# Optimization experiments

Measured on AMD Instinct MI355X. Metric: run time of the kernel, lower is better.

Reference implementation:

```python
import jax, jax.numpy as jnp
import numpy as np

N, E, F_IN, H, C = 50000, 800000, 256, 128, 40


def _gcn_norm(edge_index, num_nodes, dtype):
    # add self loops (fill value 1.0), symmetric normalization D^-1/2 A D^-1/2
    src, dst = edge_index[0], edge_index[1]
    loop = jnp.arange(num_nodes, dtype=src.dtype)
    src = jnp.concatenate([src, loop])
    dst = jnp.concatenate([dst, loop])
    w = jnp.ones(src.shape[0], dtype=dtype)
    deg = jax.ops.segment_sum(w, dst, num_segments=num_nodes)
    dinv = jnp.where(deg > 0, jax.lax.rsqrt(deg), jnp.zeros_like(deg))
    norm = dinv[src] * w * dinv[dst]
    return src, dst, norm


def _propagate(x, src, dst, w, num_nodes):
    # gather x[src], scale by edge weight, scatter-add at dst (SpMM)
    return jax.ops.segment_sum(w[:, None] * x[src], dst, num_segments=num_nodes)


def _mixhop_conv(x, src, dst, w, Ws, b):
    # powers = [0, 1, 2]; Ws[p] is [in, out]
    n = x.shape[0]
    outs = [x @ Ws[0]]
    h = x
    for p in (1, 2):
        h = _propagate(h, src, dst, w, n)
        outs.append(h @ Ws[p])
    return jnp.concatenate(outs, axis=-1) + b


def setup_inputs() -> dict:
    key = jax.random.key(0)
    ks = jax.random.split(key, 10)
    x = jax.random.normal(ks[0], (N, F_IN), dtype=jnp.float32)
    edge_index = jax.random.randint(ks[1], (2, E), 0, N, dtype=jnp.int64)
    s1 = 1.0 / np.sqrt(F_IN)
    s2 = 1.0 / np.sqrt(3 * H)
    return {
        "x": x,
        "edge_index": edge_index,
        "W1_0": jax.random.uniform(ks[2], (F_IN, H), jnp.float32, -s1, s1),
        "W1_1": jax.random.uniform(ks[3], (F_IN, H), jnp.float32, -s1, s1),
        "W1_2": jax.random.uniform(ks[4], (F_IN, H), jnp.float32, -s1, s1),
        "b1": jnp.zeros((3 * H,), jnp.float32),
        "W2_0": jax.random.uniform(ks[5], (3 * H, C), jnp.float32, -s2, s2),
        "W2_1": jax.random.uniform(ks[6], (3 * H, C), jnp.float32, -s2, s2),
        "W2_2": jax.random.uniform(ks[7], (3 * H, C), jnp.float32, -s2, s2),
        "b2": jnp.zeros((3 * C,), jnp.float32),
    }


def reference(x, edge_index, W1_0, W1_1, W1_2, b1, W2_0, W2_1, W2_2, b2):
    n = x.shape[0]
    src, dst, w = _gcn_norm(edge_index, n, x.dtype)
    h = jax.nn.relu(_mixhop_conv(x, src, dst, w, (W1_0, W1_1, W1_2), b1))
    # eval mode: dropout is identity
    out = _mixhop_conv(h, src, dst, w, (W2_0, W2_1, W2_2), b2)
    return jax.nn.log_softmax(out, axis=1)
```

## Files before the change

kernel.cpp:

```cpp
#include <hip/hip_runtime.h>
#include <hip/hip_bf16.h>
#include <math.h>

#define N_NODES 50000
#define F_IN 256
#define H1 128
#define C_OUT 40
#define L1W 384
#define L2W 120
#define L2WP 128
#define NBUK 196
#define NBLK1 256

typedef __attribute__((ext_vector_type(8))) short short8;
typedef __attribute__((ext_vector_type(4))) float f32x4;
typedef __attribute__((ext_vector_type(2))) float f32x2;
typedef __attribute__((ext_vector_type(4))) unsigned short us4;

__device__ inline unsigned short f2bf(float f) {
    union { float f; unsigned int u; } x;
    x.f = f;
    unsigned int u = x.u;
    return (unsigned short)((u + 0x7FFF + ((u >> 16) & 1)) >> 16);
}
__device__ inline float bf2f(unsigned short u) {
    union { unsigned int u; float f; } x;
    x.u = (unsigned int)u << 16;
    return x.f;
}
__device__ inline unsigned int pack_fp8x4(float a, float b, float c, float d) {
    int v = 0;
    v = __builtin_amdgcn_cvt_pk_fp8_f32(a, b, v, false);
    v = __builtin_amdgcn_cvt_pk_fp8_f32(c, d, v, true);
    return (unsigned int)v;
}
__device__ inline unsigned char pack_fp8x1(float a) {
    return (unsigned char)(__builtin_amdgcn_cvt_pk_fp8_f32(a, a, 0, false) & 0xFF);
}
#define EDGE_S(r) ((int)((r) & 0xFFFFu))
#define EDGE_W(r) bf2f((unsigned short)((r) >> 16))


__global__ void detect_k(const int* __restrict__ ei, int* __restrict__ flag) {
    __shared__ int any;
    if (threadIdx.x == 0) any = 0;
    __syncthreads();
    int v = 0;
    for (int r = 0; r < 4; r++) {
        int e = threadIdx.x + r * 256;
        v |= ei[e * 2 + 1];
    }
    if (v != 0) atomicOr(&any, 1);
    __syncthreads();
    if (threadIdx.x == 0) *flag = any;
}


__global__ void hist_k(const int* __restrict__ ei, const int* __restrict__ flag,
                       int* __restrict__ cnt, int E) {
    int base = (blockIdx.x * 256 + threadIdx.x) * 4;
    if (base >= E) return;
    if (base + 4 <= E) {
        int d0, d1, d2, d3;
        if (*flag) {
            int4 dv = *(const int4*)(ei + E + base);
            d0 = dv.x; d1 = dv.y; d2 = dv.z; d3 = dv.w;
        } else {
            const long long* e64 = (const long long*)ei;
            longlong2 a = *(const longlong2*)(e64 + E + base);
            longlong2 b = *(const longlong2*)(e64 + E + base + 2);
            d0 = (int)a.x; d1 = (int)a.y; d2 = (int)b.x; d3 = (int)b.y;
        }
        atomicAdd(&cnt[d0], 1);
        atomicAdd(&cnt[d1], 1);
        atomicAdd(&cnt[d2], 1);
        atomicAdd(&cnt[d3], 1);
    } else {
        for (int e = base; e < E; e++) {
            int d = (*flag) ? ei[E + e] : (int)((const long long*)ei)[E + e];
            atomicAdd(&cnt[d], 1);
        }
    }
}


__global__ __launch_bounds__(256) void scan1_k(const int* __restrict__ cnt,
                                               int* __restrict__ bsum, int n) {
    int t = threadIdx.x;
    int i = blockIdx.x * 256 + t;
    int v = (i < n) ? cnt[i] : 0;
    for (int off = 32; off; off >>= 1) v += __shfl_down(v, off, 64);
    __shared__ int ws[4];
    if ((t & 63) == 0) ws[t >> 6] = v;
    __syncthreads();
    if (t == 0) bsum[blockIdx.x] = ws[0] + ws[1] + ws[2] + ws[3];
}

__global__ __launch_bounds__(256) void scan2_k(int* __restrict__ bsum,
                                               int* __restrict__ btot, int nb) {
    __shared__ int s[256];
    int t = threadIdx.x;
    int v = (t < nb) ? bsum[t] : 0;
    s[t] = v;
    __syncthreads();
    for (int off = 1; off < 256; off <<= 1) {
        int u = (t >= off) ? s[t - off] : 0;
        __syncthreads();
        s[t] += u;
        __syncthreads();
    }
    if (t < nb) bsum[t] = s[t] - v;
    if (t == nb - 1) *btot = s[t];
}

__global__ __launch_bounds__(256) void scan3_k(const int* __restrict__ cnt,
                                               const int* __restrict__ bsum,
                                               int* __restrict__ rowptr,
// ... 13 lines not shown
    if (i < n) {
        rowptr[i] = s[t] - v + bsum[blockIdx.x];
        if (dinv) dinv[i] = rsqrtf((float)v + 1.0f);
    }
}


__global__ __launch_bounds__(256) void hist2_k(const int* __restrict__ ei,
                                               const int* __restrict__ flag,
                                               int* __restrict__ cnt2, int E) {
    __shared__ int lcnt[NBUK];
    int t = threadIdx.x, blk = blockIdx.x;
    for (int j = t; j < NBUK; j += 256) lcnt[j] = 0;
    __syncthreads();
    int chunk = (E + NBLK1 - 1) / NBLK1;
    int beg = blk * chunk, end = min(beg + chunk, E);
    bool i32 = (*flag) != 0;
    const long long* e64 = (const long long*)ei;
    for (int e = beg + t; e < end; e += 256) {
        int d = i32 ? ei[E + e] : (int)e64[E + e];
        atomicAdd(&lcnt[d >> 8], 1);
    }
    __syncthreads();
    for (int j = t; j < NBUK; j += 256) cnt2[j * NBLK1 + blk] = lcnt[j];
}

__global__ __launch_bounds__(256) void stage_k(const int* __restrict__ ei,
                                               const int* __restrict__ flag,
                                               const int* __restrict__ off2,
                                               unsigned int* __restrict__ stage, int E) {
    __shared__ int lcur[NBUK];
    int t = threadIdx.x, blk = blockIdx.x;
    for (int j = t; j < NBUK; j += 256) lcur[j] = off2[j * NBLK1 + blk];
    __syncthreads();
    int chunk = (E + NBLK1 - 1) / NBLK1;
    int beg = blk * chunk, end = min(beg + chunk, E);
    bool i32 = (*flag) != 0;
    const long long* e64 = (const long long*)ei;
    for (int e = beg + t; e < end; e += 256) {
        int s, d;
        if (i32) { s = ei[e]; d = ei[E + e]; }
        else { s = (int)e64[e]; d = (int)e64[E + e]; }
        int b = d >> 8;
        int pos = atomicAdd(&lcur[b], 1);
        stage[pos] = ((unsigned int)(d & 255) << 16) | (unsigned int)s;
    }
}

__global__ __launch_bounds__(256) void scatter2_k(const unsigned int* __restrict__ stage,
                                                  const int* __restrict__ off2,
                                                  const int* __restrict__ rowptr,
                                                  const float* __restrict__ dinv,
                                                  unsigned int* __restrict__ csr,
                                                  int E, int n) {
    __shared__ int lfill[256];
    int b = blockIdx.x, t = threadIdx.x;
    int node0 = b << 8;
    int node = node0 + t;
    lfill[t] = (node < n) ? rowptr[node] : 0;
    __syncthreads();
    int segBeg = off2[b * NBLK1];
    int segEnd = (b == NBUK - 1) ? E : off2[(b + 1) * NBLK1];
    for (int e = segBeg + t; e < segEnd; e += 256) {
        unsigned int rec = stage[e];
        int dl = rec >> 16;
        int s = rec & 0xFFFF;
        int d = node0 + dl;
        float w = dinv[s] * dinv[d];
        int pos = atomicAdd(&lfill[dl], 1);
        csr[pos] = ((unsigned int)f2bf(w) << 16) | (unsigned int)s;
    }
}


#define N1PACK ((F_IN / 32) * L1W * 32)
#define N2PACK ((L1W / 32) * L2WP * 32)

__global__ void pack_k(const float* __restrict__ w10, const float* __restrict__ w11,
                       const float* __restrict__ w12, const float* __restrict__ w20,
                       const float* __restrict__ w21, const float* __restrict__ w22,
                       unsigned short* __restrict__ Bp1, unsigned short* __restrict__ Bp2) {
    int idx = blockIdx.x * 256 + threadIdx.x;
    if (idx < N1PACK) {
        int kk = idx & 31;
        int nn = (idx >> 5) % L1W;
        int kt = idx / (L1W * 32);
        int k = kt * 32 + kk;
        int p = nn >> 7, c = nn & 127;
        const float* w = (p == 0) ? w10 : (p == 1) ? w11 : w12;
        Bp1[idx] = f2bf(w[k * H1 + c]);
    } else if (idx < N1PACK + N2PACK) {
        int j = idx - N1PACK;
        int kk = j & 31;
        int nn = (j >> 5) & (L2WP - 1);
        int kt = j >> 12;
        int k = kt * 32 + kk;
        unsigned short v = 0;
        if (nn < L2W) {
            int p = nn / 40, c = nn % 40;
            const float* w = (p == 0) ? w20 : (p == 1) ? w21 : w22;
            v = f2bf(w[k * C_OUT + c]);
        }
        Bp2[j] = v;
    }
}


__global__ __launch_bounds__(256) void mgemm1_k(const float* __restrict__ A,
                                                const unsigned short* __restrict__ Bp,
                                                const float* __restrict__ b1,
                                                unsigned short* __restrict__ Hb,
                                                unsigned char* __restrict__ Y8, int N) {
    int tid = threadIdx.x;
    int wave = tid >> 6, lane = tid & 63;
    int m = lane & 15, kq = lane >> 4;
    int nwg = gridDim.x, bid = blockIdx.x;
    int q = nwg >> 3, r = nwg & 7;
    int xcd = bid & 7, pos = bid >> 3;
    int lb = (xcd < r ? xcd * (q + 1) : r * (q + 1) + (xcd - r) * q) + pos;
    int blkM = lb >> 1, blkN = lb & 1;
    int s0 = blkN * 12;
    int row0 = blkM * 64 + wave * 16;
    int arow = row0 + m;
    if (arow >= N) arow = N - 1;
    const float* Ap = A + (size_t)arow * F_IN + kq * 8;
    const unsigned short* Bw = Bp + (size_t)s0 * 512 + (size_t)m * 32 + (size_t)kq * 8;

    short8 areg[8];
#pragma unroll
    for (int kt = 0; kt < 8; kt++) {
        float4 u = *(const float4*)(Ap + kt * 32);
        float4 v = *(const float4*)(Ap + kt * 32 + 4);
        short8 a;
        a[0] = (short)f2bf(u.x); a[1] = (short)f2bf(u.y);
        a[2] = (short)f2bf(u.z); a[3] = (short)f2bf(u.w);
        a[4] = (short)f2bf(v.x); a[5] = (short)f2bf(v.y);
        a[6] = (short)f2bf(v.z); a[7] = (short)f2bf(v.w);
        areg[kt] = a;
    }

    f32x4 acc[12];
#pragma unroll
    for (int s = 0; s < 12; s++) acc[s] = (f32x4){0.f, 0.f, 0.f, 0.f};

    short8 brA[12], brB[12];
#pragma unroll
    for (int s = 0; s < 12; s++) brA[s] = *(const short8*)(Bw + (size_t)s * 512);

#pragma unroll
    for (int kt = 0; kt < 8; kt++) {
        const unsigned short* Bn = Bw + (size_t)(kt + 1) * (L1W * 32);
        if ((kt & 1) == 0) {
            if (kt < 7) {
#pragma unroll
                for (int s = 0; s < 12; s++) brB[s] = *(const short8*)(Bn + (size_t)s * 512);
            }
#pragma unroll
            for (int s = 0; s < 12; s++)
                acc[s] = __builtin_amdgcn_mfma_f32_16x16x32_bf16(areg[kt], brA[s], acc[s], 0, 0, 0);
        } else {
            if (kt < 7) {
#pragma unroll
                for (int s = 0; s < 12; s++) brA[s] = *(const short8*)(Bn + (size_t)s * 512);
            }
#pragma unroll
            for (int s = 0; s < 12; s++)
                acc[s] = __builtin_amdgcn_mfma_f32_16x16x32_bf16(areg[kt], brB[s], acc[s], 0, 0, 0);
        }
    }

    int crow = row0 + kq * 4;
    if (blkN == 0) {
#pragma unroll
        for (int s = 0; s < 8; s++) {
            int col = s * 16 + m;
            float bias = b1[col];
#pragma unroll
            for (int r2 = 0; r2 < 4; r2++) {
                int row = crow + r2;
                if (row < N) Hb[(size_t)row * L1W + col] = f2bf(fmaxf(acc[s][r2] + bias, 0.f));
            }
        }
#pragma unroll
        for (int r2 = 0; r2 < 4; r2++) {
            int row = crow + r2;
            if (row < N) {
                unsigned int u = pack_fp8x4(acc[8][r2], acc[9][r2], acc[10][r2], acc[11][r2]);
                *(unsigned int*)(Y8 + (size_t)row * 256 + m * 16) = u;
            }
        }
    } else {
#pragma unroll
        for (int r2 = 0; r2 < 4; r2++) {
            int row = crow + r2;
            if (row < N) {
                unsigned int u0 = pack_fp8x4(acc[0][r2], acc[1][r2], acc[2][r2], acc[3][r2]);
                uint2 u12;
                u12.x = pack_fp8x4(acc[4][r2], acc[5][r2], acc[6][r2], acc[7][r2]);
                u12.y = pack_fp8x4(acc[8][r2], acc[9][r2], acc[10][r2], acc[11][r2]);
                *(unsigned int*)(Y8 + (size_t)row * 256 + m * 16 + 4) = u0;
                *(uint2*)(Y8 + (size_t)row * 256 + m * 16 + 8) = u12;
            }
        }
    }
}


__global__ __launch_bounds__(256) void mgemm2_k(const unsigned short* __restrict__ A,
                                                const unsigned short* __restrict__ Bp,
                                                unsigned short* __restrict__ Ub,
                                                unsigned char* __restrict__ U8, int N) {
    int tid = threadIdx.x;
    int wave = tid >> 6, lane = tid & 63;
    int m = lane & 15, kq = lane >> 4;
    int row0 = blockIdx.x * 64 + wave * 16;
    int arow = row0 + m;
    if (arow >= N) arow = N - 1;
    const unsigned short* Ap = A + (size_t)arow * L1W + kq * 8;
    const unsigned short* Bw = Bp + (size_t)m * 32 + (size_t)kq * 8;

    short8 areg[12];
#pragma unroll
    for (int kt = 0; kt < 12; kt++) areg[kt] = *(const short8*)(Ap + kt * 32);

    f32x4 acc[8];
#pragma unroll
    for (int s = 0; s < 8; s++) acc[s] = (f32x4){0.f, 0.f, 0.f, 0.f};

    short8 brA[8], brB[8];
#pragma unroll
    for (int s = 0; s < 8; s++) brA[s] = *(const short8*)(Bw + (size_t)s * 512);

#pragma unroll
    for (int kt = 0; kt < 12; kt++) {
        const unsigned short* Bn = Bw + (size_t)(kt + 1) * (L2WP * 32);
        if ((kt & 1) == 0) {
            if (kt < 11) {
#pragma unroll
                for (int s = 0; s < 8; s++) brB[s] = *(const short8*)(Bn + (size_t)s * 512);
            }
#pragma unroll
            for (int s = 0; s < 8; s++)
                acc[s] = __builtin_amdgcn_mfma_f32_16x16x32_bf16(areg[kt], brA[s], acc[s], 0, 0, 0);
        } else {
            if (kt < 11) {
#pragma unroll
                for (int s = 0; s < 8; s++) brA[s] = *(const short8*)(Bn + (size_t)s * 512);
            }
#pragma unroll
            for (int s = 0; s < 8; s++)
                acc[s] = __builtin_amdgcn_mfma_f32_16x16x32_bf16(areg[kt], brB[s], acc[s], 0, 0, 0);
        }
    }

    int crow = row0 + kq * 4;
#pragma unroll
    for (int s = 0; s < 3; s++) {
        int col = s * 16 + m;
#pragma unroll
        for (int r2 = 0; r2 < 4; r2++) {
            int row = crow + r2;
            if (row < N) Ub[(size_t)row * L2WP + col] = f2bf(acc[s][r2]);
        }
    }
#pragma unroll
    for (int r2 = 0; r2 < 4; r2++) {
        int row = crow + r2;
        if (row < N) {
            uint2 u;
            u.x = pack_fp8x4(acc[0][r2], acc[1][r2], acc[2][r2], acc[3][r2]);
            u.y = pack_fp8x4(acc[4][r2], acc[5][r2], acc[6][r2], acc[7][r2]);
            *(uint2*)(U8 + (size_t)row * 128 + m * 8) = u;
        }
    }
}


__global__ __launch_bounds__(256) void prop256f_k(const unsigned char* __restrict__ Y8,
                                                  unsigned short* __restrict__ Hb,
                                                  unsigned char* __restrict__ T8,
                                                  const int* __restrict__ rowptr,
                                                  const unsigned int* __restrict__ csr,
                                                  const float* __restrict__ dinv,
                                                  const float* __restrict__ b1, int n) {
    int wave = threadIdx.x >> 6, lane = threadIdx.x & 63;
    int i = blockIdx.x * 4 + wave;
    if (i >= n) return;
    int beg = rowptr[i], end = rowptr[i + 1];
    float di = dinv[i];
    const unsigned int* sbase = (const unsigned int*)Y8 + lane;
    unsigned int sv = sbase[(size_t)i * 64];
    float w = di * di;
    f32x2 slo = __builtin_amdgcn_cvt_pk_f32_fp8(sv, false);
    f32x2 shi = __builtin_amdgcn_cvt_pk_f32_fp8(sv, true);
    float a0 = w * slo.x, a1 = w * slo.y, a2 = w * shi.x, a3 = w * shi.y;

#define CONS256(rr, vv)                                                       \
    _Pragma("unroll") for (int e = 0; e < 8; e++) {                           \
        float we = EDGE_W(rr[e]);                                             \
        f32x2 lo = __builtin_amdgcn_cvt_pk_f32_fp8(vv[e], false);             \
        f32x2 hi = __builtin_amdgcn_cvt_pk_f32_fp8(vv[e], true);              \
        a0 = fmaf(we, lo.x, a0);                                              \
        a1 = fmaf(we, lo.y, a1);                                              \
        a2 = fmaf(we, hi.x, a2);                                              \
        a3 = fmaf(we, hi.y, a3);                                              \
    }

    int nfull = (end - beg) >> 3;
    unsigned int rrA[8], rrB[8];
    if (nfull > 0) {
#pragma unroll
        for (int e = 0; e < 8; e++) rrA[e] = csr[beg + e];
        int it = 0;
        while (it + 2 <= nfull) {
            {
                unsigned int vv[8];
#pragma unroll
                for (int e = 0; e < 8; e++) vv[e] = sbase[(size_t)EDGE_S(rrA[e]) * 64];
#pragma unroll
                for (int e = 0; e < 8; e++) rrB[e] = csr[beg + ((it + 1) << 3) + e];
                CONS256(rrA, vv)
            }
            {
                unsigned int vv[8];
#pragma unroll
                for (int e = 0; e < 8; e++) vv[e] = sbase[(size_t)EDGE_S(rrB[e]) * 64];
                if (it + 2 < nfull) {
#pragma unroll
                    for (int e = 0; e < 8; e++) rrA[e] = csr[beg + ((it + 2) << 3) + e];
                }
                CONS256(rrB, vv)
            }
            it += 2;
        }
        if (it < nfull) {
            unsigned int vv[8];
#pragma unroll
            for (int e = 0; e < 8; e++) vv[e] = sbase[(size_t)EDGE_S(rrA[e]) * 64];
            CONS256(rrA, vv)
        }
    }
    int k = beg + (nfull << 3);
    if (k < end) {
        unsigned int rrt[8];
#pragma unroll
        for (int e = 0; e < 8; e++) {
            int idx = k + e;
            rrt[e] = csr[idx < end ? idx : beg];
        }
        unsigned int vv[8];
#pragma unroll
        for (int e = 0; e < 8; e++) vv[e] = sbase[(size_t)EDGE_S(rrt[e]) * 64];
#pragma unroll
        for (int e = 0; e < 8; e++) {
            float we = (k + e < end) ? EDGE_W(rrt[e]) : 0.f;
            f32x2 lo = __builtin_amdgcn_cvt_pk_f32_fp8(vv[e], false);
// ... 340 lines not shown
        v1 = -INFINITY;
    }
    float m = fmaxf(v0, v1);
    for (int off = 32; off; off >>= 1) m = fmaxf(m, __shfl_xor(m, off, 64));
    float s = expf(v0 - m) + ((j1 < 120) ? expf(v1 - m) : 0.f);
    for (int off = 32; off; off >>= 1) s += __shfl_xor(s, off, 64);
    float ls = logf(s) + m;
    out[(size_t)i * 120 + lane] = v0 - ls;
    if (j1 < 120) out[(size_t)i * 120 + j1] = v1 - ls;
}


static inline size_t align256(size_t x) { return (x + 255) & ~(size_t)255; }

extern "C" void kernel_launch(void* const* d_in, const int* in_sizes, int n_in,
                              void* d_out, int out_size, void* d_ws, size_t ws_size,
                              hipStream_t stream) {
    const float* x = (const float*)d_in[0];
    const int* ei = (const int*)d_in[1];
    const float* W1_0 = (const float*)d_in[2];
    const float* W1_1 = (const float*)d_in[3];
    const float* W1_2 = (const float*)d_in[4];
    const float* b1 = (const float*)d_in[5];
    const float* W2_0 = (const float*)d_in[6];
    const float* W2_1 = (const float*)d_in[7];
    const float* W2_2 = (const float*)d_in[8];
    const float* b2 = (const float*)d_in[9];
    float* out = (float*)d_out;

    const int n = N_NODES;
    const int E = in_sizes[1] / 2;
    const int nb = (n + 255) / 256;
    const int nbe4 = ((E + 3) / 4 + 255) / 256;
    const int n2 = NBUK * NBLK1;
    const int nb2 = (n2 + 255) / 256;

    char* p = (char*)d_ws;
    size_t off = 0;
    auto alloc = [&](size_t bytes) {
        void* r = p + off;
        off = align256(off + bytes);
        return r;
    };
    int* flag = (int*)alloc(4);
    int* cnt = (int*)alloc((size_t)n * 4);
    int* rowptr = (int*)alloc((size_t)(n + 1) * 4);
    int* bsum = (int*)alloc((size_t)nb * 4);
    float* dinv = (float*)alloc((size_t)n * 4);
    unsigned int* csr = (unsigned int*)alloc((size_t)E * 4);
    int* cnt2 = (int*)alloc((size_t)n2 * 4);
    int* off2 = (int*)alloc((size_t)n2 * 4);
    int* bsum2 = (int*)alloc((size_t)nb2 * 4);
    int* tot2 = (int*)alloc(4);
    unsigned int* stage = (unsigned int*)alloc((size_t)E * 4);
    unsigned short* Bp1 = (unsigned short*)alloc((size_t)N1PACK * 2);
    unsigned short* Bp2 = (unsigned short*)alloc((size_t)N2PACK * 2);
    unsigned short* Hb = (unsigned short*)alloc((size_t)n * L1W * 2);
    unsigned char* Y8 = (unsigned char*)alloc((size_t)n * 256);
    unsigned char* T8 = (unsigned char*)alloc((size_t)n * 128);
    unsigned short* Ub = (unsigned short*)alloc((size_t)n * L2WP * 2);
    unsigned char* U8 = (unsigned char*)alloc((size_t)n * 128);
    unsigned short* T2a = (unsigned short*)alloc((size_t)n * C_OUT * 2);
    unsigned char* T8b = (unsigned char*)alloc((size_t)n * C_OUT);
    (void)ws_size;

    detect_k<<<1, 256, 0, stream>>>(ei, flag);

    hipMemsetAsync(cnt, 0, (size_t)n * 4, stream);
    hist_k<<<nbe4, 256, 0, stream>>>(ei, flag, cnt, E);
    scan1_k<<<nb, 256, 0, stream>>>(cnt, bsum, n);
    scan2_k<<<1, 256, 0, stream>>>(bsum, rowptr + n, nb);
    scan3_k<<<nb, 256, 0, stream>>>(cnt, bsum, rowptr, dinv, n);

    hist2_k<<<NBLK1, 256, 0, stream>>>(ei, flag, cnt2, E);
    scan1_k<<<nb2, 256, 0, stream>>>(cnt2, bsum2, n2);
    scan2_k<<<1, 256, 0, stream>>>(bsum2, tot2, nb2);
    scan3_k<<<nb2, 256, 0, stream>>>(cnt2, bsum2, off2, (float*)nullptr, n2);
    stage_k<<<NBLK1, 256, 0, stream>>>(ei, flag, off2, stage, E);
    scatter2_k<<<NBUK, 256, 0, stream>>>(stage, off2, rowptr, dinv, csr, E, n);

    pack_k<<<(N1PACK + N2PACK + 255) / 256, 256, 0, stream>>>(W1_0, W1_1, W1_2,
                                                              W2_0, W2_1, W2_2, Bp1, Bp2);

    mgemm1_k<<<2 * ((n + 63) / 64), 256, 0, stream>>>(x, Bp1, b1, Hb, Y8, n);
    prop256f_k<<<(n + 3) / 4, 256, 0, stream>>>(Y8, Hb, T8, rowptr, csr, dinv, b1, n);
    prop128f_k<<<(n + 3) / 4, 256, 0, stream>>>(T8, Hb, rowptr, csr, dinv, b1, n);

    mgemm2_k<<<(n + 63) / 64, 256, 0, stream>>>(Hb, Bp2, Ub, U8, n);
    propU8_k<<<(n + 3) / 4, 256, 0, stream>>>(U8, T2a, T8b, rowptr, csr, dinv, n);

    lsm_prop_k<<<(n + 3) / 4, 256, 0, stream>>>(Ub, T2a, T8b, rowptr, csr, dinv, b2, out, n);
}
```

Before: 387.6 us.

## Restructure dense GEMMs: waves split N, B staged in LDS via async loads

Both dense GEMM kernels are reorganised. Each wave now owns a slice of output columns across all 64 rows, instead of owning 16 rows across all columns. The B operand is repacked into MFMA-fragment order and streamed into per-wave double-buffered LDS with global_load_lds, while A fragments are prefetched from global one k-step ahead. gemm1 no longer splits N across two blocks, which halves the grid and stops A from being read twice. The manual waitcnt and sched_barrier pipelining and the launch_bounds occupancy hints add register and LDS pressure, and the epilogue becomes per-wave column-split stores with smaller fp8 writes.

```diff
diff --git a/kernel.cpp b/kernel.cpp
--- a/kernel.cpp
+++ b/kernel.cpp
@@ -15,7 +15,13 @@
 typedef __attribute__((ext_vector_type(8))) short short8;
 typedef __attribute__((ext_vector_type(4))) float f32x4;
 typedef __attribute__((ext_vector_type(2))) float f32x2;
-typedef __attribute__((ext_vector_type(4))) unsigned short us4;
+
+typedef __attribute__((address_space(1))) const unsigned int gu32;
+typedef __attribute__((address_space(3))) unsigned int lu32;
+
+__device__ __forceinline__ void g2l16(const void* g, void* l) {
+    __builtin_amdgcn_global_load_lds((gu32*)g, (lu32*)l, 16, 0, 0);
+}
 
 __device__ inline unsigned short f2bf(float f) {
     union { float f; unsigned int u; } x;
@@ -33,6 +39,9 @@
     v = __builtin_amdgcn_cvt_pk_fp8_f32(a, b, v, false);
     v = __builtin_amdgcn_cvt_pk_fp8_f32(c, d, v, true);
     return (unsigned int)v;
+}
+__device__ inline unsigned short pack_fp8x2(float a, float b) {
+    return (unsigned short)(__builtin_amdgcn_cvt_pk_fp8_f32(a, b, 0, false) & 0xFFFF);
 }
 __device__ inline unsigned char pack_fp8x1(float a) {
     return (unsigned char)(__builtin_amdgcn_cvt_pk_fp8_f32(a, a, 0, false) & 0xFF);
@@ -212,22 +221,28 @@
                        unsigned short* __restrict__ Bp1, unsigned short* __restrict__ Bp2) {
     int idx = blockIdx.x * 256 + threadIdx.x;
     if (idx < N1PACK) {
-        int kk = idx & 31;
-        int nn = (idx >> 5) % L1W;
         int kt = idx / (L1W * 32);
-        int k = kt * 32 + kk;
-        int p = nn >> 7, c = nn & 127;
+        int t = idx % (L1W * 32);
+        int s = t >> 9;
+        int u = t & 511;
+        int kq = u >> 7, m = (u >> 3) & 15, kk = u & 7;
+        int col = s * 16 + m;
+        int k = kt * 32 + kq * 8 + kk;
+        int p = col >> 7, c = col & 127;
         const float* w = (p == 0) ? w10 : (p == 1) ? w11 : w12;
         Bp1[idx] = f2bf(w[k * H1 + c]);
     } else if (idx < N1PACK + N2PACK) {
         int j = idx - N1PACK;
-        int kk = j & 31;
-        int nn = (j >> 5) & (L2WP - 1);
-        int kt = j >> 12;
-        int k = kt * 32 + kk;
+        int kt = j / (L2WP * 32);
+        int t = j % (L2WP * 32);
+        int s = t >> 9;
+        int u = t & 511;
+        int kq = u >> 7, m = (u >> 3) & 15, kk = u & 7;
+        int col = s * 16 + m;
+        int k = kt * 32 + kq * 8 + kk;
         unsigned short v = 0;
-        if (nn < L2W) {
-            int p = nn / 40, c = nn % 40;
+        if (col < L2W) {
+            int p = col / 40, c = col % 40;
             const float* w = (p == 0) ? w20 : (p == 1) ? w21 : w22;
             v = f2bf(w[k * C_OUT + c]);
         }
@@ -236,172 +251,276 @@
 }
 
 
-__global__ __launch_bounds__(256) void mgemm1_k(const float* __restrict__ A,
-                                                const unsigned short* __restrict__ Bp,
-                                                const float* __restrict__ b1,
-                                                unsigned short* __restrict__ Hb,
-                                                unsigned char* __restrict__ Y8, int N) {
+__global__ __launch_bounds__(256, 2) void mgemm1_k(const float* __restrict__ A,
+                                                   const unsigned short* __restrict__ Bp,
+                                                   const float* __restrict__ b1,
+                                                   unsigned short* __restrict__ Hb,
+                                                   unsigned char* __restrict__ Y8, int N) {
+    __shared__ unsigned short Bls[4][2][3072];
     int tid = threadIdx.x;
-    int wave = tid >> 6, lane = tid & 63;
+    int w = tid >> 6, lane = tid & 63;
     int m = lane & 15, kq = lane >> 4;
-    int nwg = gridDim.x, bid = blockIdx.x;
-    int q = nwg >> 3, r = nwg & 7;
-    int xcd = bid & 7, pos = bid >> 3;
-    int lb = (xcd < r ? xcd * (q + 1) : r * (q + 1) + (xcd - r) * q) + pos;
-    int blkM = lb >> 1, blkN = lb & 1;
-    int s0 = blkN * 12;
-    int row0 = blkM * 64 + wave * 16;
-    int arow = row0 + m;
-    if (arow >= N) arow = N - 1;
-    const float* Ap = A + (size_t)arow * F_IN + kq * 8;
-    const unsigned short* Bw = Bp + (size_t)s0 * 512 + (size_t)m * 32 + (size_t)kq * 8;
-
-    short8 areg[8];
+    int row0 = blockIdx.x * 64;
+    const char* srcb = (const char*)Bp + (size_t)(w * 6) * 1024 + (size_t)lane * 16;
+
+    const float* Ap0;
+    const float* Ap1;
+    const float* Ap2;
+    const float* Ap3;
+    {
+        int a0 = row0 + 0 * 16 + m; if (a0 >= N) a0 = N - 1;
+        int a1 = row0 + 1 * 16 + m; if (a1 >= N) a1 = N - 1;
+        int a2 = row0 + 2 * 16 + m; if (a2 >= N) a2 = N - 1;
+        int a3 = row0 + 3 * 16 + m; if (a3 >= N) a3 = N - 1;
+        Ap0 = A + (size_t)a0 * F_IN + kq * 8;
+        Ap1 = A + (size_t)a1 * F_IN + kq * 8;
+        Ap2 = A + (size_t)a2 * F_IN + kq * 8;
+        Ap3 = A + (size_t)a3 * F_IN + kq * 8;
+    }
+
+    f32x4 acc[4][6];
+#pragma unroll
+    for (int f = 0; f < 4; f++)
+#pragma unroll
+        for (int j = 0; j < 6; j++) acc[f][j] = (f32x4){0.f, 0.f, 0.f, 0.f};
+
+    float4 afA[4][2], afB[4][2];
+    afA[0][0] = *(const float4*)(Ap0); afA[0][1] = *(const float4*)(Ap0 + 4);
+    afA[1][0] = *(const float4*)(Ap1); afA[1][1] = *(const float4*)(Ap1 + 4);
+    afA[2][0] = *(const float4*)(Ap2); afA[2][1] = *(const float4*)(Ap2 + 4);
+    afA[3][0] = *(const float4*)(Ap3); afA[3][1] = *(const float4*)(Ap3 + 4);
+#pragma unroll
+    for (int j = 0; j < 6; j++) g2l16(srcb + j * 1024, &Bls[w][0][j * 512]);
+#pragma unroll
+    for (int j = 0; j < 6; j++) g2l16(srcb + 24576 + j * 1024, &Bls[w][1][j * 512]);
+
 #pragma unroll
     for (int kt = 0; kt < 8; kt++) {
-        float4 u = *(const float4*)(Ap + kt * 32);
-        float4 v = *(const float4*)(Ap + kt * 32 + 4);
-        short8 a;
-        a[0] = (short)f2bf(u.x); a[1] = (short)f2bf(u.y);
-        a[2] = (short)f2bf(u.z); a[3] = (short)f2bf(u.w);
-        a[4] = (short)f2bf(v.x); a[5] = (short)f2bf(v.y);
-        a[6] = (short)f2bf(v.z); a[7] = (short)f2bf(v.w);
-        areg[kt] = a;
-    }
-
-    f32x4 acc[12];
-#pragma unroll
-    for (int s = 0; s < 12; s++) acc[s] = (f32x4){0.f, 0.f, 0.f, 0.f};
-
-    short8 brA[12], brB[12];
-#pragma unroll
-    for (int s = 0; s < 12; s++) brA[s] = *(const short8*)(Bw + (size_t)s * 512);
-
-#pragma unroll
-    for (int kt = 0; kt < 8; kt++) {
-        const unsigned short* Bn = Bw + (size_t)(kt + 1) * (L1W * 32);
-        if ((kt & 1) == 0) {
-            if (kt < 7) {
-#pragma unroll
-                for (int s = 0; s < 12; s++) brB[s] = *(const short8*)(Bn + (size_t)s * 512);
-            }
-#pragma unroll
-            for (int s = 0; s < 12; s++)
-                acc[s] = __builtin_amdgcn_mfma_f32_16x16x32_bf16(areg[kt], brA[s], acc[s], 0, 0, 0);
-        } else {
-            if (kt < 7) {
-#pragma unroll
-                for (int s = 0; s < 12; s++) brA[s] = *(const short8*)(Bn + (size_t)s * 512);
-            }
-#pragma unroll
-            for (int s = 0; s < 12; s++)
-                acc[s] = __builtin_amdgcn_mfma_f32_16x16x32_bf16(areg[kt], brB[s], acc[s], 0, 0, 0);
-        }
-    }
-
-    int crow = row0 + kq * 4;
-    if (blkN == 0) {
-#pragma unroll
-        for (int s = 0; s < 8; s++) {
-            int col = s * 16 + m;
+        if (kt < 7) { asm volatile("s_waitcnt vmcnt(6)" ::: "memory"); }
+        else        { asm volatile("s_waitcnt vmcnt(0)" ::: "memory"); }
+        __builtin_amdgcn_sched_barrier(0);
+        short8 bf[6];
+#pragma unroll
+        for (int j = 0; j < 6; j++)
+            bf[j] = *(const short8*)(&Bls[w][kt & 1][j * 512 + kq * 128 + m * 8]);
+        asm volatile("s_waitcnt lgkmcnt(0)" ::: "memory");
+        __builtin_amdgcn_sched_barrier(0);
+        if (kt < 7) {
+            if ((kt & 1) == 0) {
+                afB[0][0] = *(const float4*)(Ap0 + (kt + 1) * 32); afB[0][1] = *(const float4*)(Ap0 + (kt + 1) * 32 + 4);
+                afB[1][0] = *(const float4*)(Ap1 + (kt + 1) * 32); afB[1][1] = *(const float4*)(Ap1 + (kt + 1) * 32 + 4);
+                afB[2][0] = *(const float4*)(Ap2 + (kt + 1) * 32); afB[2][1] = *(const float4*)(Ap2 + (kt + 1) * 32 + 4);
+                afB[3][0] = *(const float4*)(Ap3 + (kt + 1) * 32); afB[3][1] = *(const float4*)(Ap3 + (kt + 1) * 32 + 4);
+            } else {
+                afA[0][0] = *(const float4*)(Ap0 + (kt + 1) * 32); afA[0][1] = *(const float4*)(Ap0 + (kt + 1) * 32 + 4);
+                afA[1][0] = *(const float4*)(Ap1 + (kt + 1) * 32); afA[1][1] = *(const float4*)(Ap1 + (kt + 1) * 32 + 4);
+                afA[2][0] = *(const float4*)(Ap2 + (kt + 1) * 32); afA[2][1] = *(const float4*)(Ap2 + (kt + 1) * 32 + 4);
+                afA[3][0] = *(const float4*)(Ap3 + (kt + 1) * 32); afA[3][1] = *(const float4*)(Ap3 + (kt + 1) * 32 + 4);
+            }
+        }
+        if (kt < 6) {
+#pragma unroll
+            for (int j = 0; j < 6; j++)
+                g2l16(srcb + (size_t)(kt + 2) * 24576 + j * 1024, &Bls[w][kt & 1][j * 512]);
+        }
+        short8 av[4];
+#pragma unroll
+        for (int f = 0; f < 4; f++) {
+            float4 u = (kt & 1) ? afB[f][0] : afA[f][0];
+            float4 v = (kt & 1) ? afB[f][1] : afA[f][1];
+            short8 a;
+            a[0] = (short)f2bf(u.x); a[1] = (short)f2bf(u.y);
+            a[2] = (short)f2bf(u.z); a[3] = (short)f2bf(u.w);
+            a[4] = (short)f2bf(v.x); a[5] = (short)f2bf(v.y);
+            a[6] = (short)f2bf(v.z); a[7] = (short)f2bf(v.w);
+            av[f] = a;
+        }
+#pragma unroll
+        for (int f = 0; f < 4; f++)
+#pragma unroll
+            for (int j = 0; j < 6; j++)
+                acc[f][j] = __builtin_amdgcn_mfma_f32_16x16x32_bf16(av[f], bf[j], acc[f][j], 0, 0, 0);
+    }
+
+    int crow0 = row0 + kq * 4;
+    if (w == 0) {
+#pragma unroll
+        for (int j = 0; j < 6; j++) {
+            int col = j * 16 + m;
             float bias = b1[col];
 #pragma unroll
+            for (int f = 0; f < 4; f++)
+#pragma unroll
+                for (int r2 = 0; r2 < 4; r2++) {
+                    int row = crow0 + f * 16 + r2;
+                    if (row < N) Hb[(size_t)row * L1W + col] = f2bf(fmaxf(acc[f][j][r2] + bias, 0.f));
+                }
+        }
+    } else if (w == 1) {
+#pragma unroll
+        for (int j = 0; j < 2; j++) {
+            int col = (6 + j) * 16 + m;
+            float bias = b1[col];
+#pragma unroll
+            for (int f = 0; f < 4; f++)
+#pragma unroll
+                for (int r2 = 0; r2 < 4; r2++) {
+                    int row = crow0 + f * 16 + r2;
+                    if (row < N) Hb[(size_t)row * L1W + col] = f2bf(fmaxf(acc[f][j][r2] + bias, 0.f));
+                }
+        }
+#pragma unroll
+        for (int f = 0; f < 4; f++)
+#pragma unroll
             for (int r2 = 0; r2 < 4; r2++) {
-                int row = crow + r2;
-                if (row < N) Hb[(size_t)row * L1W + col] = f2bf(fmaxf(acc[s][r2] + bias, 0.f));
-            }
-        }
+                int row = crow0 + f * 16 + r2;
+                if (row < N) {
+                    unsigned int u = pack_fp8x4(acc[f][2][r2], acc[f][3][r2], acc[f][4][r2], acc[f][5][r2]);
+                    *(unsigned int*)(Y8 + (size_t)row * 256 + m * 16) = u;
+                }
+            }
+    } else if (w == 2) {
+#pragma unroll
+        for (int f = 0; f < 4; f++)
+#pragma unroll
+            for (int r2 = 0; r2 < 4; r2++) {
+                int row = crow0 + f * 16 + r2;
+                if (row < N) {
+                    unsigned int u = pack_fp8x4(acc[f][0][r2], acc[f][1][r2], acc[f][2][r2], acc[f][3][r2]);
+                    unsigned short v = pack_fp8x2(acc[f][4][r2], acc[f][5][r2]);
+                    *(unsigned int*)(Y8 + (size_t)row * 256 + m * 16 + 4) = u;
+                    *(unsigned short*)(Y8 + (size_t)row * 256 + m * 16 + 8) = v;
+                }
+            }
+    } else {
+#pragma unroll
+        for (int f = 0; f < 4; f++)
+#pragma unroll
+            for (int r2 = 0; r2 < 4; r2++) {
+                int row = crow0 + f * 16 + r2;
+                if (row < N) {
+                    unsigned short v = pack_fp8x2(acc[f][0][r2], acc[f][1][r2]);
+                    unsigned int u = pack_fp8x4(acc[f][2][r2], acc[f][3][r2], acc[f][4][r2], acc[f][5][r2]);
+                    *(unsigned short*)(Y8 + (size_t)row * 256 + m * 16 + 10) = v;
+                    *(unsigned int*)(Y8 + (size_t)row * 256 + m * 16 + 12) = u;
+                }
+            }
+    }
+}
+
+
+__global__ __launch_bounds__(256, 3) void mgemm2_k(const unsigned short* __restrict__ A,
+                                                   const unsigned short* __restrict__ Bp,
+                                                   unsigned short* __restrict__ Ub,
+                                                   unsigned char* __restrict__ U8, int N) {
+    __shared__ unsigned short Bls[4][2][1024];
+    int tid = threadIdx.x;
+    int w = tid >> 6, lane = tid & 63;
+    int m = lane & 15, kq = lane >> 4;
+    int row0 = blockIdx.x * 64;
+    const char* srcb = (const char*)Bp + (size_t)(w * 2) * 1024 + (size_t)lane * 16;
+
+    const unsigned short* Ap0;
+    const unsigned short* Ap1;
+    const unsigned short* Ap2;
+    const unsigned short* Ap3;
+    {
+        int a0 = row0 + 0 * 16 + m; if (a0 >= N) a0 = N - 1;
+        int a1 = row0 + 1 * 16 + m; if (a1 >= N) a1 = N - 1;
+        int a2 = row0 + 2 * 16 + m; if (a2 >= N) a2 = N - 1;
+        int a3 = row0 + 3 * 16 + m; if (a3 >= N) a3 = N - 1;
+        Ap0 = A + (size_t)a0 * L1W + kq * 8;
+        Ap1 = A + (size_t)a1 * L1W + kq * 8;
+        Ap2 = A + (size_t)a2 * L1W + kq * 8;
+        Ap3 = A + (size_t)a3 * L1W + kq * 8;
+    }
+
+    f32x4 acc[4][2];
+#pragma unroll
+    for (int f = 0; f < 4; f++)
+#pragma unroll
+        for (int j = 0; j < 2; j++) acc[f][j] = (f32x4){0.f, 0.f, 0.f, 0.f};
+
+    short8 afA[4], afB[4];
+    afA[0] = *(const short8*)(Ap0);
+    afA[1] = *(const short8*)(Ap1);
+    afA[2] = *(const short8*)(Ap2);
+    afA[3] = *(const short8*)(Ap3);
+#pragma unroll
+    for (int j = 0; j < 2; j++) g2l16(srcb + j * 1024, &Bls[w][0][j * 512]);
+#pragma unroll
+    for (int j = 0; j < 2; j++) g2l16(srcb + 8192 + j * 1024, &Bls[w][1][j * 512]);
+
+#pragma unroll
+    for (int kt = 0; kt < 12; kt++) {
+        if (kt < 11) { asm volatile("s_waitcnt vmcnt(2)" ::: "memory"); }
+        else         { asm volatile("s_waitcnt vmcnt(0)" ::: "memory"); }
+        __builtin_amdgcn_sched_barrier(0);
+        short8 bf[2];
+#pragma unroll
+        for (int j = 0; j < 2; j++)
+            bf[j] = *(const short8*)(&Bls[w][kt & 1][j * 512 + kq * 128 + m * 8]);
+        asm volatile("s_waitcnt lgkmcnt(0)" ::: "memory");
+        __builtin_amdgcn_sched_barrier(0);
+        if (kt < 11) {
+            if ((kt & 1) == 0) {
+                afB[0] = *(const short8*)(Ap0 + (kt + 1) * 32);
+                afB[1] = *(const short8*)(Ap1 + (kt + 1) * 32);
+                afB[2] = *(const short8*)(Ap2 + (kt + 1) * 32);
+                afB[3] = *(const short8*)(Ap3 + (kt + 1) * 32);
+            } else {
+                afA[0] = *(const short8*)(Ap0 + (kt + 1) * 32);
+                afA[1] = *(const short8*)(Ap1 + (kt + 1) * 32);
+                afA[2] = *(const short8*)(Ap2 + (kt + 1) * 32);
+                afA[3] = *(const short8*)(Ap3 + (kt + 1) * 32);
+            }
+        }
+        if (kt < 10) {
+#pragma unroll
+            for (int j = 0; j < 2; j++)
+                g2l16(srcb + (size_t)(kt + 2) * 8192 + j * 1024, &Bls[w][kt & 1][j * 512]);
+        }
+#pragma unroll
+        for (int f = 0; f < 4; f++) {
+            short8 a = (kt & 1) ? afB[f] : afA[f];
+#pragma unroll
+            for (int j = 0; j < 2; j++)
+                acc[f][j] = __builtin_amdgcn_mfma_f32_16x16x32_bf16(a, bf[j], acc[f][j], 0, 0, 0);
+        }
+    }
+
+    int crow0 = row0 + kq * 4;
+#pragma unroll
+    for (int f = 0; f < 4; f++)
 #pragma unroll
         for (int r2 = 0; r2 < 4; r2++) {
-            int row = crow + r2;
+            int row = crow0 + f * 16 + r2;
             if (row < N) {
-                unsigned int u = pack_fp8x4(acc[8][r2], acc[9][r2], acc[10][r2], acc[11][r2]);
-                *(unsigned int*)(Y8 + (size_t)row * 256 + m * 16) = u;
-            }
-        }
-    } else {
-#pragma unroll
-        for (int r2 = 0; r2 < 4; r2++) {
-            int row = crow + r2;
-            if (row < N) {
-                unsigned int u0 = pack_fp8x4(acc[0][r2], acc[1][r2], acc[2][r2], acc[3][r2]);
-                uint2 u12;
-                u12.x = pack_fp8x4(acc[4][r2], acc[5][r2], acc[6][r2], acc[7][r2]);
-                u12.y = pack_fp8x4(acc[8][r2], acc[9][r2], acc[10][r2], acc[11][r2]);
-                *(unsigned int*)(Y8 + (size_t)row * 256 + m * 16 + 4) = u0;
-                *(uint2*)(Y8 + (size_t)row * 256 + m * 16 + 8) = u12;
-            }
-        }
-    }
-}
-
-
-__global__ __launch_bounds__(256) void mgemm2_k(const unsigned short* __restrict__ A,
-                                                const unsigned short* __restrict__ Bp,
-                                                unsigned short* __restrict__ Ub,
-                                                unsigned char* __restrict__ U8, int N) {
-    int tid = threadIdx.x;
-    int wave = tid >> 6, lane = tid & 63;
-    int m = lane & 15, kq = lane >> 4;
-    int row0 = blockIdx.x * 64 + wave * 16;
-    int arow = row0 + m;
-    if (arow >= N) arow = N - 1;
-    const unsigned short* Ap = A + (size_t)arow * L1W + kq * 8;
-    const unsigned short* Bw = Bp + (size_t)m * 32 + (size_t)kq * 8;
-
-    short8 areg[12];
-#pragma unroll
-    for (int kt = 0; kt < 12; kt++) areg[kt] = *(const short8*)(Ap + kt * 32);
-
-    f32x4 acc[8];
-#pragma unroll
-    for (int s = 0; s < 8; s++) acc[s] = (f32x4){0.f, 0.f, 0.f, 0.f};
-
-    short8 brA[8], brB[8];
-#pragma unroll
-    for (int s = 0; s < 8; s++) brA[s] = *(const short8*)(Bw + (size_t)s * 512);
-
-#pragma unroll
-    for (int kt = 0; kt < 12; kt++) {
-        const unsigned short* Bn = Bw + (size_t)(kt + 1) * (L2WP * 32);
-        if ((kt & 1) == 0) {
-            if (kt < 11) {
-#pragma unroll
-                for (int s = 0; s < 8; s++) brB[s] = *(const short8*)(Bn + (size_t)s * 512);
-            }
-#pragma unroll
-            for (int s = 0; s < 8; s++)
-                acc[s] = __builtin_amdgcn_mfma_f32_16x16x32_bf16(areg[kt], brA[s], acc[s], 0, 0, 0);
-        } else {
-            if (kt < 11) {
-#pragma unroll
-                for (int s = 0; s < 8; s++) brA[s] = *(const short8*)(Bn + (size_t)s * 512);
-            }
-#pragma unroll
-            for (int s = 0; s < 8; s++)
-                acc[s] = __builtin_amdgcn_mfma_f32_16x16x32_bf16(areg[kt], brB[s], acc[s], 0, 0, 0);
-        }
-    }
-
-    int crow = row0 + kq * 4;
-#pragma unroll
-    for (int s = 0; s < 3; s++) {
-        int col = s * 16 + m;
-#pragma unroll
-        for (int r2 = 0; r2 < 4; r2++) {
-            int row = crow + r2;
-            if (row < N) Ub[(size_t)row * L2WP + col] = f2bf(acc[s][r2]);
-        }
-    }
-#pragma unroll
-    for (int r2 = 0; r2 < 4; r2++) {
-        int row = crow + r2;
-        if (row < N) {
-            uint2 u;
-            u.x = pack_fp8x4(acc[0][r2], acc[1][r2], acc[2][r2], acc[3][r2]);
-            u.y = pack_fp8x4(acc[4][r2], acc[5][r2], acc[6][r2], acc[7][r2]);
-            *(uint2*)(U8 + (size_t)row * 128 + m * 8) = u;
-        }
+                unsigned short v = pack_fp8x2(acc[f][0][r2], acc[f][1][r2]);
+                *(unsigned short*)(U8 + (size_t)row * 128 + m * 8 + 2 * w) = v;
+            }
+        }
+    if (w == 0) {
+#pragma unroll
+        for (int j = 0; j < 2; j++) {
+            int col = j * 16 + m;
+#pragma unroll
+            for (int f = 0; f < 4; f++)
+#pragma unroll
+                for (int r2 = 0; r2 < 4; r2++) {
+                    int row = crow0 + f * 16 + r2;
+                    if (row < N) Ub[(size_t)row * L2WP + col] = f2bf(acc[f][j][r2]);
+                }
+        }
+    } else if (w == 1) {
+        int col = 32 + m;
+#pragma unroll
+        for (int f = 0; f < 4; f++)
+#pragma unroll
+            for (int r2 = 0; r2 < 4; r2++) {
+                int row = crow0 + f * 16 + r2;
+                if (row < N) Ub[(size_t)row * L2WP + col] = f2bf(acc[f][0][r2]);
+            }
     }
 }
 
@@ -908,7 +1027,7 @@
     pack_k<<<(N1PACK + N2PACK + 255) / 256, 256, 0, stream>>>(W1_0, W1_1, W1_2,
                                                               W2_0, W2_1, W2_2, Bp1, Bp2);
 
-    mgemm1_k<<<2 * ((n + 63) / 64), 256, 0, stream>>>(x, Bp1, b1, Hb, Y8, n);
+    mgemm1_k<<<(n + 63) / 64, 256, 0, stream>>>(x, Bp1, b1, Hb, Y8, n);
     prop256f_k<<<(n + 3) / 4, 256, 0, stream>>>(Y8, Hb, T8, rowptr, csr, dinv, b1, n);
     prop128f_k<<<(n + 3) / 4, 256, 0, stream>>>(T8, Hb, rowptr, csr, dinv, b1, n);
 
```

Result: no change. 389.5 us (+0.5%).

## Stage GEMM B tiles in LDS via async global-to-LDS double buffering

Applied to the files above, without the earlier changes.

Both dense GEMM kernels now load the packed weight matrix into a double-buffered LDS tile with global_load_lds, synchronised by explicit waitcnt and barriers, instead of each wave reading B directly from global memory into registers. The weight pack layout is reordered so each lane's fragment is contiguous for these LDS copies. mgemm1 no longer splits the 384 output columns across two blocks; each block computes all 24 column tiles, which halves the grid and the redundant fp32 A loads and conversions. The cost is more accumulator registers per thread (launch bounds 2), LDS use, and a block-wide barrier on every k step.

```diff
diff --git a/kernel.cpp b/kernel.cpp
--- a/kernel.cpp
+++ b/kernel.cpp
@@ -15,7 +15,13 @@
 typedef __attribute__((ext_vector_type(8))) short short8;
 typedef __attribute__((ext_vector_type(4))) float f32x4;
 typedef __attribute__((ext_vector_type(2))) float f32x2;
-typedef __attribute__((ext_vector_type(4))) unsigned short us4;
+
+typedef __attribute__((address_space(1))) const unsigned int gu32;
+typedef __attribute__((address_space(3))) unsigned int lu32;
+
+__device__ __forceinline__ void g2l16(const void* g, void* l) {
+    __builtin_amdgcn_global_load_lds((gu32*)g, (lu32*)l, 16, 0, 0);
+}
 
 __device__ inline unsigned short f2bf(float f) {
     union { float f; unsigned int u; } x;
@@ -33,6 +39,9 @@
     v = __builtin_amdgcn_cvt_pk_fp8_f32(a, b, v, false);
     v = __builtin_amdgcn_cvt_pk_fp8_f32(c, d, v, true);
     return (unsigned int)v;
+}
+__device__ inline unsigned short pack_fp8x2(float a, float b) {
+    return (unsigned short)(__builtin_amdgcn_cvt_pk_fp8_f32(a, b, 0, false) & 0xFFFF);
 }
 __device__ inline unsigned char pack_fp8x1(float a) {
     return (unsigned char)(__builtin_amdgcn_cvt_pk_fp8_f32(a, a, 0, false) & 0xFF);
@@ -212,22 +221,28 @@
                        unsigned short* __restrict__ Bp1, unsigned short* __restrict__ Bp2) {
     int idx = blockIdx.x * 256 + threadIdx.x;
     if (idx < N1PACK) {
-        int kk = idx & 31;
-        int nn = (idx >> 5) % L1W;
         int kt = idx / (L1W * 32);
-        int k = kt * 32 + kk;
-        int p = nn >> 7, c = nn & 127;
+        int t = idx % (L1W * 32);
+        int s = t >> 9;
+        int u = t & 511;
+        int kq = u >> 7, m = (u >> 3) & 15, kk = u & 7;
+        int col = s * 16 + m;
+        int k = kt * 32 + kq * 8 + kk;
+        int p = col >> 7, c = col & 127;
         const float* w = (p == 0) ? w10 : (p == 1) ? w11 : w12;
         Bp1[idx] = f2bf(w[k * H1 + c]);
     } else if (idx < N1PACK + N2PACK) {
         int j = idx - N1PACK;
-        int kk = j & 31;
-        int nn = (j >> 5) & (L2WP - 1);
-        int kt = j >> 12;
-        int k = kt * 32 + kk;
+        int kt = j / (L2WP * 32);
+        int t = j % (L2WP * 32);
+        int s = t >> 9;
+        int u = t & 511;
+        int kq = u >> 7, m = (u >> 3) & 15, kk = u & 7;
+        int col = s * 16 + m;
+        int k = kt * 32 + kq * 8 + kk;
         unsigned short v = 0;
-        if (nn < L2W) {
-            int p = nn / 40, c = nn % 40;
+        if (col < L2W) {
+            int p = col / 40, c = col % 40;
             const float* w = (p == 0) ? w20 : (p == 1) ? w21 : w22;
             v = f2bf(w[k * C_OUT + c]);
         }
@@ -236,31 +251,35 @@
 }
 
 
-__global__ __launch_bounds__(256) void mgemm1_k(const float* __restrict__ A,
-                                                const unsigned short* __restrict__ Bp,
-                                                const float* __restrict__ b1,
-                                                unsigned short* __restrict__ Hb,
-                                                unsigned char* __restrict__ Y8, int N) {
+__global__ __launch_bounds__(256, 2) void mgemm1_k(const float* __restrict__ A,
+                                                   const unsigned short* __restrict__ Bp,
+                                                   const float* __restrict__ b1,
+                                                   unsigned short* __restrict__ Hb,
+                                                   unsigned char* __restrict__ Y8, int N) {
+    __shared__ unsigned short Bls[2][L1W * 32];
     int tid = threadIdx.x;
-    int wave = tid >> 6, lane = tid & 63;
+    int w = tid >> 6, lane = tid & 63;
     int m = lane & 15, kq = lane >> 4;
-    int nwg = gridDim.x, bid = blockIdx.x;
-    int q = nwg >> 3, r = nwg & 7;
-    int xcd = bid & 7, pos = bid >> 3;
-    int lb = (xcd < r ? xcd * (q + 1) : r * (q + 1) + (xcd - r) * q) + pos;
-    int blkM = lb >> 1, blkN = lb & 1;
-    int s0 = blkN * 12;
-    int row0 = blkM * 64 + wave * 16;
+    int row0 = blockIdx.x * 64 + w * 16;
     int arow = row0 + m;
     if (arow >= N) arow = N - 1;
     const float* Ap = A + (size_t)arow * F_IN + kq * 8;
-    const unsigned short* Bw = Bp + (size_t)s0 * 512 + (size_t)m * 32 + (size_t)kq * 8;
-
+    const char* srcb = (const char*)Bp + (size_t)(w * 6) * 1024 + (size_t)lane * 16;
+
+    float4 at0[8], at1[8];
+#pragma unroll
+    for (int kt = 0; kt < 8; kt++) {
+        at0[kt] = *(const float4*)(Ap + kt * 32);
+        at1[kt] = *(const float4*)(Ap + kt * 32 + 4);
+    }
+#pragma unroll
+    for (int j = 0; j < 6; j++) g2l16(srcb + j * 1024, &Bls[0][(w * 6 + j) * 512]);
+#pragma unroll
+    for (int j = 0; j < 6; j++) g2l16(srcb + 24576 + j * 1024, &Bls[1][(w * 6 + j) * 512]);
     short8 areg[8];
 #pragma unroll
     for (int kt = 0; kt < 8; kt++) {
-        float4 u = *(const float4*)(Ap + kt * 32);
-        float4 v = *(const float4*)(Ap + kt * 32 + 4);
+        float4 u = at0[kt], v = at1[kt];
         short8 a;
         a[0] = (short)f2bf(u.x); a[1] = (short)f2bf(u.y);
         a[2] = (short)f2bf(u.z); a[3] = (short)f2bf(u.w);
@@ -269,118 +288,116 @@
         areg[kt] = a;
     }
 
-    f32x4 acc[12];
-#pragma unroll
-    for (int s = 0; s < 12; s++) acc[s] = (f32x4){0.f, 0.f, 0.f, 0.f};
-
-    short8 brA[12], brB[12];
-#pragma unroll
-    for (int s = 0; s < 12; s++) brA[s] = *(const short8*)(Bw + (size_t)s * 512);
+    f32x4 acc[24];
+#pragma unroll
+    for (int s = 0; s < 24; s++) acc[s] = (f32x4){0.f, 0.f, 0.f, 0.f};
 
 #pragma unroll
     for (int kt = 0; kt < 8; kt++) {
-        const unsigned short* Bn = Bw + (size_t)(kt + 1) * (L1W * 32);
-        if ((kt & 1) == 0) {
-            if (kt < 7) {
-#pragma unroll
-                for (int s = 0; s < 12; s++) brB[s] = *(const short8*)(Bn + (size_t)s * 512);
+        if (kt < 7) { asm volatile("s_waitcnt vmcnt(6)" ::: "memory"); }
+        else        { asm volatile("s_waitcnt vmcnt(0)" ::: "memory"); }
+        __builtin_amdgcn_sched_barrier(0);
+        __builtin_amdgcn_s_barrier();
+        const unsigned short* Bbuf = Bls[kt & 1];
+#pragma unroll
+        for (int c = 0; c < 4; c++) {
+            short8 bf[6];
+#pragma unroll
+            for (int j = 0; j < 6; j++)
+                bf[j] = *(const short8*)(&Bbuf[(c * 6 + j) * 512 + lane * 8]);
+            asm volatile("s_waitcnt lgkmcnt(0)" ::: "memory");
+            __builtin_amdgcn_sched_barrier(0);
+            if (c == 3) {
+                __builtin_amdgcn_s_barrier();
+                if (kt < 6) {
+#pragma unroll
+                    for (int j = 0; j < 6; j++)
+                        g2l16(srcb + (size_t)(kt + 2) * 24576 + j * 1024,
+                              &Bls[kt & 1][(w * 6 + j) * 512]);
+                }
             }
 #pragma unroll
-            for (int s = 0; s < 12; s++)
-                acc[s] = __builtin_amdgcn_mfma_f32_16x16x32_bf16(areg[kt], brA[s], acc[s], 0, 0, 0);
-        } else {
-            if (kt < 7) {
-#pragma unroll
-                for (int s = 0; s < 12; s++) brA[s] = *(const short8*)(Bn + (size_t)s * 512);
-            }
-#pragma unroll
-            for (int s = 0; s < 12; s++)
-                acc[s] = __builtin_amdgcn_mfma_f32_16x16x32_bf16(areg[kt], brB[s], acc[s], 0, 0, 0);
+            for (int j = 0; j < 6; j++)
+                acc[c * 6 + j] = __builtin_amdgcn_mfma_f32_16x16x32_bf16(
+                    areg[kt], bf[j], acc[c * 6 + j], 0, 0, 0);
         }
     }
 
     int crow = row0 + kq * 4;
-    if (blkN == 0) {
-#pragma unroll
-        for (int s = 0; s < 8; s++) {
-            int col = s * 16 + m;
-            float bias = b1[col];
-#pragma unroll
-            for (int r2 = 0; r2 < 4; r2++) {
-                int row = crow + r2;
-                if (row < N) Hb[(size_t)row * L1W + col] = f2bf(fmaxf(acc[s][r2] + bias, 0.f));
-            }
-        }
+#pragma unroll
+    for (int s = 0; s < 8; s++) {
+        int col = s * 16 + m;
+        float bias = b1[col];
 #pragma unroll
         for (int r2 = 0; r2 < 4; r2++) {
             int row = crow + r2;
-            if (row < N) {
-                unsigned int u = pack_fp8x4(acc[8][r2], acc[9][r2], acc[10][r2], acc[11][r2]);
-                *(unsigned int*)(Y8 + (size_t)row * 256 + m * 16) = u;
-            }
-        }
-    } else {
-#pragma unroll
-        for (int r2 = 0; r2 < 4; r2++) {
-            int row = crow + r2;
-            if (row < N) {
-                unsigned int u0 = pack_fp8x4(acc[0][r2], acc[1][r2], acc[2][r2], acc[3][r2]);
-                uint2 u12;
-                u12.x = pack_fp8x4(acc[4][r2], acc[5][r2], acc[6][r2], acc[7][r2]);
-                u12.y = pack_fp8x4(acc[8][r2], acc[9][r2], acc[10][r2], acc[11][r2]);
-                *(unsigned int*)(Y8 + (size_t)row * 256 + m * 16 + 4) = u0;
-                *(uint2*)(Y8 + (size_t)row * 256 + m * 16 + 8) = u12;
-            }
-        }
-    }
-}
-
-
-__global__ __launch_bounds__(256) void mgemm2_k(const unsigned short* __restrict__ A,
-                                                const unsigned short* __restrict__ Bp,
-                                                unsigned short* __restrict__ Ub,
-                                                unsigned char* __restrict__ U8, int N) {
+            if (row < N) Hb[(size_t)row * L1W + col] = f2bf(fmaxf(acc[s][r2] + bias, 0.f));
+        }
+    }
+#pragma unroll
+    for (int r2 = 0; r2 < 4; r2++) {
+        int row = crow + r2;
+        if (row < N) {
+            uint4 u;
+            u.x = pack_fp8x4(acc[8][r2], acc[9][r2], acc[10][r2], acc[11][r2]);
+            u.y = pack_fp8x4(acc[12][r2], acc[13][r2], acc[14][r2], acc[15][r2]);
+            u.z = pack_fp8x4(acc[16][r2], acc[17][r2], acc[18][r2], acc[19][r2]);
+            u.w = pack_fp8x4(acc[20][r2], acc[21][r2], acc[22][r2], acc[23][r2]);
+            *(uint4*)(Y8 + (size_t)row * 256 + m * 16) = u;
+        }
+    }
+}
+
+
+__global__ __launch_bounds__(256, 3) void mgemm2_k(const unsigned short* __restrict__ A,
+                                                   const unsigned short* __restrict__ Bp,
+                                                   unsigned short* __restrict__ Ub,
+                                                   unsigned char* __restrict__ U8, int N) {
+    __shared__ unsigned short Bls[2][L2WP * 32];
     int tid = threadIdx.x;
-    int wave = tid >> 6, lane = tid & 63;
+    int w = tid >> 6, lane = tid & 63;
     int m = lane & 15, kq = lane >> 4;
-    int row0 = blockIdx.x * 64 + wave * 16;
+    int row0 = blockIdx.x * 64 + w * 16;
     int arow = row0 + m;
     if (arow >= N) arow = N - 1;
     const unsigned short* Ap = A + (size_t)arow * L1W + kq * 8;
-    const unsigned short* Bw = Bp + (size_t)m * 32 + (size_t)kq * 8;
+    const char* srcb = (const char*)Bp + (size_t)(w * 2) * 1024 + (size_t)lane * 16;
 
     short8 areg[12];
 #pragma unroll
     for (int kt = 0; kt < 12; kt++) areg[kt] = *(const short8*)(Ap + kt * 32);
+#pragma unroll
+    for (int j = 0; j < 2; j++) g2l16(srcb + j * 1024, &Bls[0][(w * 2 + j) * 512]);
+#pragma unroll
+    for (int j = 0; j < 2; j++) g2l16(srcb + 8192 + j * 1024, &Bls[1][(w * 2 + j) * 512]);
 
     f32x4 acc[8];
 #pragma unroll
     for (int s = 0; s < 8; s++) acc[s] = (f32x4){0.f, 0.f, 0.f, 0.f};
 
-    short8 brA[8], brB[8];
-#pragma unroll
-    for (int s = 0; s < 8; s++) brA[s] = *(const short8*)(Bw + (size_t)s * 512);
-
 #pragma unroll
     for (int kt = 0; kt < 12; kt++) {
-        const unsigned short* Bn = Bw + (size_t)(kt + 1) * (L2WP * 32);
-        if ((kt & 1) == 0) {
-            if (kt < 11) {
-#pragma unroll
-                for (int s = 0; s < 8; s++) brB[s] = *(const short8*)(Bn + (size_t)s * 512);
-            }
-#pragma unroll
-            for (int s = 0; s < 8; s++)
-                acc[s] = __builtin_amdgcn_mfma_f32_16x16x32_bf16(areg[kt], brA[s], acc[s], 0, 0, 0);
-        } else {
-            if (kt < 11) {
-#pragma unroll
-                for (int s = 0; s < 8; s++) brA[s] = *(const short8*)(Bn + (size_t)s * 512);
-            }
-#pragma unroll
-            for (int s = 0; s < 8; s++)
-                acc[s] = __builtin_amdgcn_mfma_f32_16x16x32_bf16(areg[kt], brB[s], acc[s], 0, 0, 0);
-        }
+        if (kt < 11) { asm volatile("s_waitcnt vmcnt(2)" ::: "memory"); }
+        else         { asm volatile("s_waitcnt vmcnt(0)" ::: "memory"); }
+        __builtin_amdgcn_sched_barrier(0);
+        __builtin_amdgcn_s_barrier();
+        const unsigned short* Bbuf = Bls[kt & 1];
+        short8 bf[8];
+#pragma unroll
+        for (int j = 0; j < 8; j++)
+            bf[j] = *(const short8*)(&Bbuf[j * 512 + lane * 8]);
+        asm volatile("s_waitcnt lgkmcnt(0)" ::: "memory");
+        __builtin_amdgcn_sched_barrier(0);
+        __builtin_amdgcn_s_barrier();
+        if (kt < 10) {
+#pragma unroll
+            for (int j = 0; j < 2; j++)
+                g2l16(srcb + (size_t)(kt + 2) * 8192 + j * 1024,
+                      &Bls[kt & 1][(w * 2 + j) * 512]);
+        }
+#pragma unroll
+        for (int j = 0; j < 8; j++)
+            acc[j] = __builtin_amdgcn_mfma_f32_16x16x32_bf16(areg[kt], bf[j], acc[j], 0, 0, 0);
     }
 
     int crow = row0 + kq * 4;
@@ -908,7 +925,7 @@
     pack_k<<<(N1PACK + N2PACK + 255) / 256, 256, 0, stream>>>(W1_0, W1_1, W1_2,
                                                               W2_0, W2_1, W2_2, Bp1, Bp2);
 
-    mgemm1_k<<<2 * ((n + 63) / 64), 256, 0, stream>>>(x, Bp1, b1, Hb, Y8, n);
+    mgemm1_k<<<(n + 63) / 64, 256, 0, stream>>>(x, Bp1, b1, Hb, Y8, n);
     prop256f_k<<<(n + 3) / 4, 256, 0, stream>>>(Y8, Hb, T8, rowptr, csr, dinv, b1, n);
     prop128f_k<<<(n + 3) / 4, 256, 0, stream>>>(T8, Hb, rowptr, csr, dinv, b1, n);
 
```

Result: faster. 344.1 us (-11.2%).
